# Kernel optimization log

Hardware: AMD Instinct MI355X
Metric: run time of the kernel (lower is better)

Reference implementation:

```python
import jax, jax.numpy as jnp
import numpy as np

B, D_IN, C, P = 8192, 2048, 1000, 256


def setup_inputs() -> dict:
    key = jax.random.key(0)
    ks = jax.random.split(key, 6)
    return {
        "x": jax.random.normal(ks[0], (B, D_IN), dtype=jnp.float32),
        "Wm": jax.random.normal(ks[1], (C, D_IN), dtype=jnp.float32) * (1.0 / np.sqrt(D_IN)),
        "bm": jax.random.normal(ks[2], (C,), dtype=jnp.float32) * 0.01,
        "u": jax.random.normal(ks[3], (P, C), dtype=jnp.float32),
        "v": jax.random.normal(ks[4], (P, C), dtype=jnp.float32),
        "w": jax.random.normal(ks[5], (P, 1), dtype=jnp.float32),
    }


def reference(x, Wm, bm, u, v, w):
    # Backbone: Linear(D_IN -> C) producing per-instance logits (B, C)
    preds = jnp.einsum("bd,cd->bc", x, Wm) + bm
    # Gated attention, fully batched (replaces per-instance Python loop):
    # tanh(u @ pred) * sigmoid(v @ pred)  -> (B, P)
    gated = jnp.tanh(jnp.einsum("bc,pc->bp", preds, u)) * jax.nn.sigmoid(
        jnp.einsum("bc,pc->bp", preds, v)
    )
    scores = (gated @ w).ravel()          # (B,)
    attention = jax.nn.softmax(scores)    # softmax over instances
    total_pred = jnp.sum(preds * attention[:, None])
    return preds, total_pred
```

## Files before the change

### kernel.cpp

```cpp
#include <hip/hip_runtime.h>
#include <hip/hip_fp16.h>

typedef _Float16 half8 __attribute__((ext_vector_type(8)));
typedef float f32x4 __attribute__((ext_vector_type(4)));

#define B_   8192
#define DIN  2048
#define C_   1000
#define CP   1024
#define NP2  512

static const size_t OFF_XH  = 0;
static const size_t OFF_WH  = OFF_XH  + (size_t)B_ * DIN * 2;
static const size_t OFF_UVH = OFF_WH  + (size_t)CP * DIN * 2;
static const size_t OFF_PH  = OFF_UVH + (size_t)NP2 * CP * 2;
static const size_t OFF_SC  = OFF_PH  + (size_t)B_ * CP * 2;
static const size_t OFF_RS  = OFF_SC  + (size_t)B_ * 4;
static const size_t WS_NEED = OFF_RS  + (size_t)B_ * 4;

__device__ __forceinline__ void gload16(const void* g, void* l) {
  __builtin_amdgcn_global_load_lds(
      (const __attribute__((address_space(1))) void*)g,
      (__attribute__((address_space(3))) void*)l, 16, 0, 0);
}

__global__ __launch_bounds__(256) void prep_kernel(
    const float* __restrict__ x, const float* __restrict__ Wm,
    const float* __restrict__ u, const float* __restrict__ v,
    _Float16* __restrict__ xh, _Float16* __restrict__ wh,
    _Float16* __restrict__ uvh, float* __restrict__ scores,
    float* __restrict__ rowsum)
{
  const long NX  = (long)B_ * DIN / 8;
  const long NW  = (long)CP * DIN / 8;
  const long NUV = (long)NP2 * CP / 8;
  const long NZ  = 2 * (long)B_ / 8;
  const long T   = NX + NW + NUV + NZ;
  for (long idx = (long)blockIdx.x * blockDim.x + threadIdx.x; idx < T;
       idx += (long)gridDim.x * blockDim.x) {
    if (idx < NX) {
      long e = idx * 8;
      float4 p0 = *(const float4*)(x + e);
      float4 p1 = *(const float4*)(x + e + 4);
      half8 h;
      h[0] = (_Float16)p0.x; h[1] = (_Float16)p0.y; h[2] = (_Float16)p0.z; h[3] = (_Float16)p0.w;
      h[4] = (_Float16)p1.x; h[5] = (_Float16)p1.y; h[6] = (_Float16)p1.z; h[7] = (_Float16)p1.w;
      *(half8*)(xh + e) = h;
    } else if (idx < NX + NW) {
      long e = (idx - NX) * 8;
      int row = (int)(e >> 11);
      half8 h;
      if (row < C_) {
        float4 p0 = *(const float4*)(Wm + e);
        float4 p1 = *(const float4*)(Wm + e + 4);
        h[0] = (_Float16)p0.x; h[1] = (_Float16)p0.y; h[2] = (_Float16)p0.z; h[3] = (_Float16)p0.w;
        h[4] = (_Float16)p1.x; h[5] = (_Float16)p1.y; h[6] = (_Float16)p1.z; h[7] = (_Float16)p1.w;
      } else {
        h = (half8)(_Float16)0.f;
      }
      *(half8*)(wh + e) = h;
    } else if (idx < NX + NW + NUV) {
      long e = (idx - NX - NW) * 8;
      int j = (int)(e >> 10);
      int k = (int)(e & 1023);
      const float* src = (j & 1) ? v : u;
      int p = j >> 1;
      half8 h;
      #pragma unroll
      for (int t = 0; t < 8; ++t) {
        int kk = k + t;
        h[t] = (kk < C_) ? (_Float16)src[(size_t)p * C_ + kk] : (_Float16)0.f;
      }
      *(half8*)(uvh + e) = h;
    } else {
      long e = (idx - NX - NW - NUV) * 8;
      float4 z = {0.f, 0.f, 0.f, 0.f};
      if (e < B_) {
        *(float4*)(scores + e) = z; *(float4*)(scores + e + 4) = z;
      } else {
        long r = e - B_;
        *(float4*)(rowsum + r) = z; *(float4*)(rowsum + r + 4) = z;
      }
    }
  }
}

__global__ __launch_bounds__(256) void gemm1_kernel(
    const _Float16* __restrict__ xh, const _Float16* __restrict__ wh,
    const float* __restrict__ bmv, float* __restrict__ preds,
    _Float16* __restrict__ predsh, float* __restrict__ rowsum)
{
  __shared__ _Float16 sA[128 * 64];
  __shared__ _Float16 sB[128 * 64];
  const int tid  = threadIdx.x;
  const int lane = tid & 63;
  const int w    = tid >> 6;
  const int wm   = w >> 1, wn = w & 1;
  const int bm0  = blockIdx.x * 128;
  const int bn0  = blockIdx.y * 128;

  f32x4 acc[4][4] = {};

  const _Float16* srcA[4]; const _Float16* srcB[4];
  _Float16* dstA[4]; _Float16* dstB[4];
  #pragma unroll
  for (int i = 0; i < 4; ++i) {
    int slot = i * 256 + tid;
    int row  = slot >> 3;
    int cb   = (slot & 7) << 4;
    int scb  = cb ^ ((row & 7) << 4);
    srcA[i] = xh + (size_t)(bm0 + row) * DIN + (scb >> 1);
    srcB[i] = wh + (size_t)(bn0 + row) * DIN + (scb >> 1);
    dstA[i] = sA + (i * 4 + w) * 512;
    dstB[i] = sB + (i * 4 + w) * 512;
  }
  int aoff[4][2], boff[4][2];
  #pragma unroll
  for (int mi = 0; mi < 4; ++mi) {
    #pragma unroll
    for (int ks = 0; ks < 2; ++ks) {
      int kb = ks * 64 + (lane >> 4) * 16;
      int ra = wm * 64 + mi * 16 + (lane & 15);
      aoff[mi][ks] = ra * 128 + (kb ^ ((ra & 7) << 4));
      int rb = wn * 64 + mi * 16 + (lane & 15);
      boff[mi][ks] = rb * 128 + (kb ^ ((rb & 7) << 4));
    }
  }

  for (int kt = 0; kt < DIN / 64; ++kt) {
    #pragma unroll
    for (int i = 0; i < 4; ++i) {
      gload16(srcA[i], dstA[i]);
      gload16(srcB[i], dstB[i]);
      srcA[i] += 64; srcB[i] += 64;
    }
    asm volatile("s_waitcnt vmcnt(0)" ::: "memory");
    __syncthreads();
    #pragma unroll
    for (int ks = 0; ks < 2; ++ks) {
      half8 a[4], b[4];
      #pragma unroll
      for (int mi = 0; mi < 4; ++mi) a[mi] = *(const half8*)((const char*)sA + aoff[mi][ks]);
      #pragma unroll
      for (int ni = 0; ni < 4; ++ni) b[ni] = *(const half8*)((const char*)sB + boff[ni][ks]);
      #pragma unroll
      for (int mi = 0; mi < 4; ++mi)
        #pragma unroll
        for (int ni = 0; ni < 4; ++ni)
          acc[mi][ni] = __builtin_amdgcn_mfma_f32_16x16x32_f16(a[mi], b[ni], acc[mi][ni], 0, 0, 0);
    }
    __syncthreads();
  }

  float rp[4][4] = {};
  #pragma unroll
  for (int mi = 0; mi < 4; ++mi) {
    #pragma unroll
    for (int ni = 0; ni < 4; ++ni) {
      f32x4 d = acc[mi][ni];
      int gc = bn0 + wn * 64 + ni * 16 + (lane & 15);
      float bias = (gc < C_) ? bmv[gc] : 0.f;
      #pragma unroll
      for (int j = 0; j < 4; ++j) {
        int gr = bm0 + wm * 64 + mi * 16 + (lane >> 4) * 4 + j;
        float val = d[j] + bias;
        predsh[(size_t)gr * CP + gc] = (_Float16)val;
        if (gc < C_) preds[(size_t)gr * C_ + gc] = val;
        rp[mi][j] += val;
      }
    }
  }
  #pragma unroll
  for (int mi = 0; mi < 4; ++mi) {
    #pragma unroll
    for (int j = 0; j < 4; ++j) {
      float s = rp[mi][j];
      s += __shfl_xor(s, 1); s += __shfl_xor(s, 2);
      s += __shfl_xor(s, 4); s += __shfl_xor(s, 8);
      if ((lane & 15) == 0) {
        int gr = bm0 + wm * 64 + mi * 16 + (lane >> 4) * 4 + j;
        atomicAdd(&rowsum[gr], s);
      }
    }
  }
}

__global__ __launch_bounds__(256) void gemm2_kernel(
    const _Float16* __restrict__ predsh, const _Float16* __restrict__ uvh,
    const float* __restrict__ wv, float* __restrict__ scores)
{
  __shared__ _Float16 sA[128 * 64];
  __shared__ _Float16 sB[128 * 64];
  const int tid  = threadIdx.x;
  const int lane = tid & 63;
  const int w    = tid >> 6;
  const int wm   = w >> 1, wn = w & 1;
  const int bm0  = blockIdx.x * 128;
  const int bn0  = blockIdx.y * 128;

  f32x4 acc[4][4] = {};

  const _Float16* srcA[4]; const _Float16* srcB[4];
  _Float16* dstA[4]; _Float16* dstB[4];
  #pragma unroll
  for (int i = 0; i < 4; ++i) {
    int slot = i * 256 + tid;
    int row  = slot >> 3;
    int cb   = (slot & 7) << 4;
    int scb  = cb ^ ((row & 7) << 4);
    srcA[i] = predsh + (size_t)(bm0 + row) * CP + (scb >> 1);
    srcB[i] = uvh    + (size_t)(bn0 + row) * CP + (scb >> 1);
    dstA[i] = sA + (i * 4 + w) * 512;
    dstB[i] = sB + (i * 4 + w) * 512;
  }
  int aoff[4][2], boff[4][2];
  #pragma unroll
  for (int mi = 0; mi < 4; ++mi) {
    #pragma unroll
    for (int ks = 0; ks < 2; ++ks) {
      int kb = ks * 64 + (lane >> 4) * 16;
      int ra = wm * 64 + mi * 16 + (lane & 15);
      aoff[mi][ks] = ra * 128 + (kb ^ ((ra & 7) << 4));
      int rb = wn * 64 + mi * 16 + (lane & 15);
      boff[mi][ks] = rb * 128 + (kb ^ ((rb & 7) << 4));
    }
  }

  for (int kt = 0; kt < CP / 64; ++kt) {
    #pragma unroll
    for (int i = 0; i < 4; ++i) {
      gload16(srcA[i], dstA[i]);
      gload16(srcB[i], dstB[i]);
      srcA[i] += 64; srcB[i] += 64;
    }
    asm volatile("s_waitcnt vmcnt(0)" ::: "memory");
    __syncthreads();
    #pragma unroll
    for (int ks = 0; ks < 2; ++ks) {
      half8 a[4], b[4];
      #pragma unroll
      for (int mi = 0; mi < 4; ++mi) a[mi] = *(const half8*)((const char*)sA + aoff[mi][ks]);
      #pragma unroll
      for (int ni = 0; ni < 4; ++ni) b[ni] = *(const half8*)((const char*)sB + boff[ni][ks]);
      #pragma unroll
      for (int mi = 0; mi < 4; ++mi)
        #pragma unroll
        for (int ni = 0; ni < 4; ++ni)
          acc[mi][ni] = __builtin_amdgcn_mfma_f32_16x16x32_f16(a[mi], b[ni], acc[mi][ni], 0, 0, 0);
    }
    __syncthreads();
  }

  float sp[4][4] = {};
  #pragma unroll
  for (int mi = 0; mi < 4; ++mi) {
    #pragma unroll
    for (int ni = 0; ni < 4; ++ni) {
      f32x4 d = acc[mi][ni];
      int gc = bn0 + wn * 64 + ni * 16 + (lane & 15);
      float wq = wv[gc >> 1];
      bool even = ((gc & 1) == 0);
      #pragma unroll
      for (int j = 0; j < 4; ++j) {
        float t  = d[j];
        float pr = __shfl_xor(t, 1);
        float th = 2.f / (1.f + __expf(-2.f * t)) - 1.f;
        float sg = 1.f / (1.f + __expf(-pr));
        sp[mi][j] += even ? (th * sg * wq) : 0.f;
      }
    }
  }
  #pragma unroll
  for (int mi = 0; mi < 4; ++mi) {
    #pragma unroll
    for (int j = 0; j < 4; ++j) {
      float s = sp[mi][j];
      s += __shfl_xor(s, 1); s += __shfl_xor(s, 2);
      s += __shfl_xor(s, 4); s += __shfl_xor(s, 8);
      if ((lane & 15) == 0) {
        int gr = bm0 + wm * 64 + mi * 16 + (lane >> 4) * 4 + j;
        atomicAdd(&scores[gr], s);
      }
    }
  }
}

__global__ __launch_bounds__(1024) void final_kernel(
    const float* __restrict__ scores, const float* __restrict__ rowsum,
    float* __restrict__ out)
{
  __shared__ float red[16], red2[16];
  const int t = threadIdx.x;
  const int lane = t & 63, wid = t >> 6;
  float s[8];
  float m = -3.4e38f;
  #pragma unroll
  for (int i = 0; i < 8; ++i) { s[i] = scores[t + i * 1024]; m = fmaxf(m, s[i]); }
  #pragma unroll
  for (int off = 1; off < 64; off <<= 1) m = fmaxf(m, __shfl_xor(m, off));
  if (lane == 0) red[wid] = m;
  __syncthreads();
  #pragma unroll
  for (int i = 0; i < 16; ++i) m = fmaxf(m, red[i]);
  __syncthreads();

  float se = 0.f, sr = 0.f;
  #pragma unroll
  for (int i = 0; i < 8; ++i) {
    float e = __expf(s[i] - m);
    se += e;
    sr += e * rowsum[t + i * 1024];
  }
  #pragma unroll
  for (int off = 1; off < 64; off <<= 1) { se += __shfl_xor(se, off); sr += __shfl_xor(sr, off); }
  if (lane == 0) { red[wid] = se; red2[wid] = sr; }
  __syncthreads();
  if (t == 0) {
    float tse = 0.f, tsr = 0.f;
    for (int i = 0; i < 16; ++i) { tse += red[i]; tsr += red2[i]; }
    out[0] = tsr / tse;
  }
}

extern "C" void kernel_launch(void* const* d_in, const int* in_sizes, int n_in,
                              void* d_out, int out_size, void* d_ws, size_t ws_size,
                              hipStream_t stream)
{
  const float* x   = (const float*)d_in[0];
  const float* Wm  = (const float*)d_in[1];
  const float* bmv = (const float*)d_in[2];
  const float* u   = (const float*)d_in[3];
  const float* v   = (const float*)d_in[4];
  const float* wv  = (const float*)d_in[5];
  float* out = (float*)d_out;

  if (ws_size < WS_NEED) return;

  char* ws = (char*)d_ws;
  _Float16* xh     = (_Float16*)(ws + OFF_XH);
  _Float16* wh     = (_Float16*)(ws + OFF_WH);
  _Float16* uvh    = (_Float16*)(ws + OFF_UVH);
  _Float16* predsh = (_Float16*)(ws + OFF_PH);
  float*    scores = (float*)(ws + OFF_SC);
  float*    rowsum = (float*)(ws + OFF_RS);

  prep_kernel<<<2048, 256, 0, stream>>>(x, Wm, u, v, xh, wh, uvh, scores, rowsum);
  gemm1_kernel<<<dim3(64, 8), 256, 0, stream>>>(xh, wh, bmv, out, predsh, rowsum);
  gemm2_kernel<<<dim3(64, 4), 256, 0, stream>>>(predsh, uvh, wv, scores);
  final_kernel<<<1, 1024, 0, stream>>>(scores, rowsum, out + (size_t)B_ * C_);
}
```

Before: 101.5 us.

## Double-buffer LDS tiles in both GEMMs and halve gemm2 M-tile

Both GEMM kernels now use two LDS buffers. The global-to-LDS load for the next K-tile is issued before computing the current one, with partial vmcnt waits and raw barriers, so memory latency overlaps with MFMA work. gemm2 also shrinks its M tile from 128 to 64 rows and doubles its grid, giving 512 blocks instead of 256 to better fill the CUs. This raises LDS use per block and moves synchronisation into hand-placed waits that must exactly match the number of outstanding loads.

Measured after the change: 95.60 us. 1.06x faster.

```diff
diff --git a/kernel.cpp b/kernel.cpp
--- a/kernel.cpp
+++ b/kernel.cpp
@@ -90,8 +90,8 @@
     const float* __restrict__ bmv, float* __restrict__ preds,
     _Float16* __restrict__ predsh, float* __restrict__ rowsum)
 {
-  __shared__ _Float16 sA[128 * 64];
-  __shared__ _Float16 sB[128 * 64];
+  __shared__ _Float16 sA[2][128 * 64];
+  __shared__ _Float16 sB[2][128 * 64];
   const int tid  = threadIdx.x;
   const int lane = tid & 63;
   const int w    = tid >> 6;
@@ -102,7 +102,6 @@
   f32x4 acc[4][4] = {};
 
   const _Float16* srcA[4]; const _Float16* srcB[4];
-  _Float16* dstA[4]; _Float16* dstB[4];
   #pragma unroll
   for (int i = 0; i < 4; ++i) {
     int slot = i * 256 + tid;
@@ -111,8 +110,6 @@
     int scb  = cb ^ ((row & 7) << 4);
     srcA[i] = xh + (size_t)(bm0 + row) * DIN + (scb >> 1);
     srcB[i] = wh + (size_t)(bn0 + row) * DIN + (scb >> 1);
-    dstA[i] = sA + (i * 4 + w) * 512;
-    dstB[i] = sB + (i * 4 + w) * 512;
   }
   int aoff[4][2], boff[4][2];
   #pragma unroll
@@ -127,29 +124,55 @@
     }
   }
 
-  for (int kt = 0; kt < DIN / 64; ++kt) {
+  auto stage = [&](int c) {
     #pragma unroll
     for (int i = 0; i < 4; ++i) {
-      gload16(srcA[i], dstA[i]);
-      gload16(srcB[i], dstB[i]);
+      gload16(srcA[i], &sA[c][(i * 4 + w) * 512]);
+      gload16(srcB[i], &sB[c][(i * 4 + w) * 512]);
       srcA[i] += 64; srcB[i] += 64;
     }
-    asm volatile("s_waitcnt vmcnt(0)" ::: "memory");
-    __syncthreads();
+  };
+
+  auto compute = [&](int c) {
+    const char* bA = (const char*)&sA[c][0];
+    const char* bB = (const char*)&sB[c][0];
     #pragma unroll
     for (int ks = 0; ks < 2; ++ks) {
       half8 a[4], b[4];
       #pragma unroll
-      for (int mi = 0; mi < 4; ++mi) a[mi] = *(const half8*)((const char*)sA + aoff[mi][ks]);
-      #pragma unroll
-      for (int ni = 0; ni < 4; ++ni) b[ni] = *(const half8*)((const char*)sB + boff[ni][ks]);
+      for (int mi = 0; mi < 4; ++mi) a[mi] = *(const half8*)(bA + aoff[mi][ks]);
+      #pragma unroll
+      for (int ni = 0; ni < 4; ++ni) b[ni] = *(const half8*)(bB + boff[ni][ks]);
       #pragma unroll
       for (int mi = 0; mi < 4; ++mi)
         #pragma unroll
         for (int ni = 0; ni < 4; ++ni)
           acc[mi][ni] = __builtin_amdgcn_mfma_f32_16x16x32_f16(a[mi], b[ni], acc[mi][ni], 0, 0, 0);
     }
-    __syncthreads();
+  };
+
+  const int NT = DIN / 64;
+  stage(0);
+  #pragma unroll 1
+  for (int kt = 0; kt < NT; kt += 2) {
+    stage(1);
+    asm volatile("s_waitcnt vmcnt(8)" ::: "memory");
+    __builtin_amdgcn_s_barrier();
+    asm volatile("" ::: "memory");
+    compute(0);
+    __builtin_amdgcn_s_barrier();
+    asm volatile("" ::: "memory");
+    if (kt + 2 < NT) {
+      stage(0);
+      asm volatile("s_waitcnt vmcnt(8)" ::: "memory");
+    } else {
+      asm volatile("s_waitcnt vmcnt(0)" ::: "memory");
+    }
+    __builtin_amdgcn_s_barrier();
+    asm volatile("" ::: "memory");
+    compute(1);
+    __builtin_amdgcn_s_barrier();
+    asm volatile("" ::: "memory");
   }
 
   float rp[4][4] = {};
@@ -189,71 +212,108 @@
     const _Float16* __restrict__ predsh, const _Float16* __restrict__ uvh,
     const float* __restrict__ wv, float* __restrict__ scores)
 {
-  __shared__ _Float16 sA[128 * 64];
-  __shared__ _Float16 sB[128 * 64];
+  __shared__ _Float16 sA[2][64 * 64];
+  __shared__ _Float16 sB[2][128 * 64];
   const int tid  = threadIdx.x;
   const int lane = tid & 63;
   const int w    = tid >> 6;
   const int wm   = w >> 1, wn = w & 1;
-  const int bm0  = blockIdx.x * 128;
+  const int bm0  = blockIdx.x * 64;
   const int bn0  = blockIdx.y * 128;
 
-  f32x4 acc[4][4] = {};
-
-  const _Float16* srcA[4]; const _Float16* srcB[4];
-  _Float16* dstA[4]; _Float16* dstB[4];
+  f32x4 acc[2][4] = {};
+
+  const _Float16* srcA[2]; const _Float16* srcB[4];
+  #pragma unroll
+  for (int i = 0; i < 2; ++i) {
+    int slot = i * 256 + tid;
+    int row  = slot >> 3;
+    int cb   = (slot & 7) << 4;
+    int scb  = cb ^ ((row & 7) << 4);
+    srcA[i] = predsh + (size_t)(bm0 + row) * CP + (scb >> 1);
+  }
   #pragma unroll
   for (int i = 0; i < 4; ++i) {
     int slot = i * 256 + tid;
     int row  = slot >> 3;
     int cb   = (slot & 7) << 4;
     int scb  = cb ^ ((row & 7) << 4);
-    srcA[i] = predsh + (size_t)(bm0 + row) * CP + (scb >> 1);
-    srcB[i] = uvh    + (size_t)(bn0 + row) * CP + (scb >> 1);
-    dstA[i] = sA + (i * 4 + w) * 512;
-    dstB[i] = sB + (i * 4 + w) * 512;
-  }
-  int aoff[4][2], boff[4][2];
-  #pragma unroll
-  for (int mi = 0; mi < 4; ++mi) {
+    srcB[i] = uvh + (size_t)(bn0 + row) * CP + (scb >> 1);
+  }
+  int aoff[2][2], boff[4][2];
+  #pragma unroll
+  for (int ks = 0; ks < 2; ++ks) {
+    int kb = ks * 64 + (lane >> 4) * 16;
+    #pragma unroll
+    for (int mi = 0; mi < 2; ++mi) {
+      int ra = wm * 32 + mi * 16 + (lane & 15);
+      aoff[mi][ks] = ra * 128 + (kb ^ ((ra & 7) << 4));
+    }
+    #pragma unroll
+    for (int ni = 0; ni < 4; ++ni) {
+      int rb = wn * 64 + ni * 16 + (lane & 15);
+      boff[ni][ks] = rb * 128 + (kb ^ ((rb & 7) << 4));
+    }
+  }
+
+  auto stage = [&](int c) {
+    #pragma unroll
+    for (int i = 0; i < 2; ++i) {
+      gload16(srcA[i], &sA[c][(i * 4 + w) * 512]);
+      srcA[i] += 64;
+    }
+    #pragma unroll
+    for (int i = 0; i < 4; ++i) {
+      gload16(srcB[i], &sB[c][(i * 4 + w) * 512]);
+      srcB[i] += 64;
+    }
+  };
+
+  auto compute = [&](int c) {
+    const char* bA = (const char*)&sA[c][0];
+    const char* bB = (const char*)&sB[c][0];
     #pragma unroll
     for (int ks = 0; ks < 2; ++ks) {
-      int kb = ks * 64 + (lane >> 4) * 16;
-      int ra = wm * 64 + mi * 16 + (lane & 15);
-      aoff[mi][ks] = ra * 128 + (kb ^ ((ra & 7) << 4));
-      int rb = wn * 64 + mi * 16 + (lane & 15);
-      boff[mi][ks] = rb * 128 + (kb ^ ((rb & 7) << 4));
-    }
-  }
-
-  for (int kt = 0; kt < CP / 64; ++kt) {
-    #pragma unroll
-    for (int i = 0; i < 4; ++i) {
-      gload16(srcA[i], dstA[i]);
-      gload16(srcB[i], dstB[i]);
-      srcA[i] += 64; srcB[i] += 64;
-    }
-    asm volatile("s_waitcnt vmcnt(0)" ::: "memory");
-    __syncthreads();
-    #pragma unroll
-    for (int ks = 0; ks < 2; ++ks) {
-      half8 a[4], b[4];
-      #pragma unroll
-      for (int mi = 0; mi < 4; ++mi) a[mi] = *(const half8*)((const char*)sA + aoff[mi][ks]);
-      #pragma unroll
-      for (int ni = 0; ni < 4; ++ni) b[ni] = *(const half8*)((const char*)sB + boff[ni][ks]);
-      #pragma unroll
-      for (int mi = 0; mi < 4; ++mi)
+      half8 a[2], b[4];
+      #pragma unroll
+      for (int mi = 0; mi < 2; ++mi) a[mi] = *(const half8*)(bA + aoff[mi][ks]);
+      #pragma unroll
+      for (int ni = 0; ni < 4; ++ni) b[ni] = *(const half8*)(bB + boff[ni][ks]);
+      #pragma unroll
+      for (int mi = 0; mi < 2; ++mi)
         #pragma unroll
         for (int ni = 0; ni < 4; ++ni)
           acc[mi][ni] = __builtin_amdgcn_mfma_f32_16x16x32_f16(a[mi], b[ni], acc[mi][ni], 0, 0, 0);
     }
-    __syncthreads();
-  }
-
-  float sp[4][4] = {};
-  #pragma unroll
-  for (int mi = 0; mi < 4; ++mi) {
+  };
+
+  const int NT = CP / 64;
+  stage(0);
+  #pragma unroll 1
+  for (int kt = 0; kt < NT; kt += 2) {
+    stage(1);
+    asm volatile("s_waitcnt vmcnt(6)" ::: "memory");
+    __builtin_amdgcn_s_barrier();
+    asm volatile("" ::: "memory");
+    compute(0);
+    __builtin_amdgcn_s_barrier();
+    asm volatile("" ::: "memory");
+    if (kt + 2 < NT) {
+      stage(0);
+      asm volatile("s_waitcnt vmcnt(6)" ::: "memory");
+    } else {
+      asm volatile("s_waitcnt vmcnt(0)" ::: "memory");
+    }
+    __builtin_amdgcn_s_barrier();
+    asm volatile("" ::: "memory");
+    compute(1);
+    __builtin_amdgcn_s_barrier();
+    asm volatile("" ::: "memory");
+  }
+
+  float sp[2][4] = {};
+  #pragma unroll
+  for (int mi = 0; mi < 2; ++mi) {
     #pragma unroll
     for (int ni = 0; ni < 4; ++ni) {
       f32x4 d = acc[mi][ni];
@@ -271,14 +331,14 @@
     }
   }
   #pragma unroll
-  for (int mi = 0; mi < 4; ++mi) {
+  for (int mi = 0; mi < 2; ++mi) {
     #pragma unroll
     for (int j = 0; j < 4; ++j) {
       float s = sp[mi][j];
       s += __shfl_xor(s, 1); s += __shfl_xor(s, 2);
       s += __shfl_xor(s, 4); s += __shfl_xor(s, 8);
       if ((lane & 15) == 0) {
-        int gr = bm0 + wm * 64 + mi * 16 + (lane >> 4) * 4 + j;
+        int gr = bm0 + wm * 32 + mi * 16 + (lane >> 4) * 4 + j;
         atomicAdd(&scores[gr], s);
       }
     }
@@ -346,6 +406,6 @@
 
   prep_kernel<<<2048, 256, 0, stream>>>(x, Wm, u, v, xh, wh, uvh, scores, rowsum);
   gemm1_kernel<<<dim3(64, 8), 256, 0, stream>>>(xh, wh, bmv, out, predsh, rowsum);
-  gemm2_kernel<<<dim3(64, 4), 256, 0, stream>>>(predsh, uvh, wv, scores);
+  gemm2_kernel<<<dim3(128, 4), 256, 0, stream>>>(predsh, uvh, wv, scores);
   final_kernel<<<1, 1024, 0, stream>>>(scores, rowsum, out + (size_t)B_ * C_);
 }
```
